# Performance work log

Measured on AMD Instinct MI355X. Metric: run time of the kernel, lower is better.

The kernel has to match this reference:

```python
import jax, jax.numpy as jnp
import numpy as np

CHUNK = 2048   # chunk_size from __init__
EPS = 1e-5     # BatchNorm eps (torch default)


def _proj(x, w, gamma, beta, mean, var):
    # 1x1 conv (no bias) + BatchNorm (eval, running stats) + ReLU
    y = jnp.einsum('bchw,oc->bohw', x, w)
    scale = gamma / jnp.sqrt(var + EPS)
    y = (y - mean[None, :, None, None]) * scale[None, :, None, None] + beta[None, :, None, None]
    return jax.nn.relu(y)


def setup_inputs() -> dict:
    key = jax.random.key(0)
    ks = jax.random.split(key, 8)
    B, Cl, Ci, Co, H, W = 2, 256, 512, 128, 128, 128
    return {
        'lidar_features': jax.random.normal(ks[0], (B, Cl, H, W), jnp.float32),
        'image_features': jax.random.normal(ks[1], (B, Ci, H, W), jnp.float32),
        # kaiming_normal fan_out for 1x1 conv: std = sqrt(2 / Co)
        'lidar_w': jax.random.normal(ks[2], (Co, Cl), jnp.float32) * np.sqrt(2.0 / Co),
        'lidar_gamma': jnp.ones((Co,), jnp.float32),
        'lidar_beta': jnp.zeros((Co,), jnp.float32),
        'lidar_mean': jax.random.normal(ks[3], (Co,), jnp.float32) * 0.1,
        'lidar_var': jax.random.uniform(ks[4], (Co,), jnp.float32, 0.5, 1.5),
        'image_w': jax.random.normal(ks[5], (Co, Ci), jnp.float32) * np.sqrt(2.0 / Co),
        'image_gamma': jnp.ones((Co,), jnp.float32),
        'image_beta': jnp.zeros((Co,), jnp.float32),
        'image_mean': jax.random.normal(ks[6], (Co,), jnp.float32) * 0.1,
        'image_var': jax.random.uniform(ks[7], (Co,), jnp.float32, 0.5, 1.5),
        'modality_weights': jnp.ones((2,), jnp.float32),
    }


def reference(lidar_features, image_features,
              lidar_w, lidar_gamma, lidar_beta, lidar_mean, lidar_var,
              image_w, image_gamma, image_beta, image_mean, image_var,
              modality_weights):
    lidar_proj = _proj(lidar_features, lidar_w, lidar_gamma, lidar_beta, lidar_mean, lidar_var)
    image_proj = _proj(image_features, image_w, image_gamma, image_beta, image_mean, image_var)
    # spatial sizes match by construction, so no interpolation branch
    B, C, H, W = lidar_proj.shape
    P = H * W
    n = P // CHUNK  # P chosen divisible by CHUNK
    # block-diagonal attention: q from image, k=v from lidar, per pixel chunk
    q = image_proj.reshape(B, C, P).transpose(0, 2, 1).reshape(B, n, CHUNK, C)
    k = lidar_proj.reshape(B, C, P).transpose(0, 2, 1).reshape(B, n, CHUNK, C)
    attn = jax.nn.softmax(jnp.einsum('bnqc,bnkc->bnqk', q, k) / jnp.sqrt(jnp.float32(C)), axis=-1)
    out = jnp.einsum('bnqk,bnkc->bnqc', attn, k)  # v == k (both are lidar_proj)
    fused = out.reshape(B, P, C).transpose(0, 2, 1).reshape(B, C, H, W)
    w = jax.nn.softmax(modality_weights)
    return w[0] * image_proj + w[1] * fused
```

## Files before the change

kernel.cpp:

```cpp
#include <hip/hip_runtime.h>
#include <hip/hip_bf16.h>

typedef __attribute__((ext_vector_type(4))) float f32x4;
typedef __attribute__((ext_vector_type(8))) short short8;

#define P_TOT 16384
#define NCO 128
#define EPS 1e-5f
#define ALPHA 0.12752269f

__device__ __forceinline__ unsigned short f2bf(float f) {
  union { float f; unsigned u; } v; v.f = f;
  unsigned r = v.u + 0x7FFFu + ((v.u >> 16) & 1u);
  return (unsigned short)(r >> 16);
}
__device__ __forceinline__ float bf2f(unsigned short h) {
  union { unsigned u; float f; } v; v.u = ((unsigned)h) << 16;
  return v.f;
}
__device__ __forceinline__ unsigned cvtpk_bf16(float lo, float hi) {
  unsigned r;
  asm("v_cvt_pk_bf16_f32 %0, %1, %2" : "=v"(r) : "v"(lo), "v"(hi));
  return r;
}
__device__ __forceinline__ void gload16(const void* g, void* l) {
  __builtin_amdgcn_global_load_lds(
      (const __attribute__((address_space(1))) unsigned*)g,
      (__attribute__((address_space(3))) unsigned*)l, 16, 0, 0);
}

__global__ __launch_bounds__(256) void proj_mfma(
    const float* __restrict__ Xl, const float* __restrict__ Xi,
    const float* __restrict__ Wl, const float* __restrict__ Wi,
    const float* __restrict__ lgm, const float* __restrict__ lbt,
    const float* __restrict__ lmn, const float* __restrict__ lvr,
    const float* __restrict__ igm, const float* __restrict__ ibt,
    const float* __restrict__ imn, const float* __restrict__ ivr,
    unsigned short* __restrict__ Lp, unsigned short* __restrict__ Ip,
    unsigned short* __restrict__ Vg)
{
  __shared__ __align__(16) char smem[36352];
  float* sc_l = (float*)(smem + 35328);
  float* sh_l = (float*)(smem + 35840);

  const int t = threadIdx.x;
  const int w = t >> 6, l = t & 63, l15 = l & 15, g = l >> 4;
  const int zz = blockIdx.y, b = zz & 1, mod = zz >> 1;
  const int pb = blockIdx.x * 128;

  const float* Xg = mod ? Xi : Xl;
  const float* Wg = mod ? Wi : Wl;
  const int Cin = mod ? 512 : 256;
  unsigned short* outp = mod ? Ip : Lp;

  if (t < 128) {
    const float* G = mod ? igm : lgm;
    const float* Bt = mod ? ibt : lbt;
    const float* M = mod ? imn : lmn;
    const float* V = mod ? ivr : lvr;
    float s = G[t] / sqrtf(V[t] + EPS);
    sc_l[t] = s;
    sh_l[t] = Bt[t] - M[t] * s;
  }

  f32x4 o[2][8];
#pragma unroll
  for (int qt = 0; qt < 2; ++qt)
#pragma unroll
    for (int nt = 0; nt < 8; ++nt) o[qt][nt] = (f32x4){0.f, 0.f, 0.f, 0.f};

  uint2 xr[8], wr[8];
  auto load_tiles = [&](int s) {
    int cc = s * 64;
#pragma unroll
    for (int i = 0; i < 8; ++i) {
      int e = t + 256 * i;
      int c = e >> 5, p4 = e & 31;
      f32x4 x = *(const f32x4*)(Xg + ((size_t)(b * Cin + cc + c)) * P_TOT + pb + p4 * 4);
      xr[i].x = cvtpk_bf16(x[0], x[1]);
      xr[i].y = cvtpk_bf16(x[2], x[3]);
    }
#pragma unroll
    for (int i = 0; i < 8; ++i) {
      int e = t + 256 * i;
      int co = e >> 4, c4 = e & 15;
      f32x4 wv = *(const f32x4*)(Wg + (size_t)co * Cin + cc + c4 * 4);
      wr[i].x = cvtpk_bf16(wv[0], wv[1]);
      wr[i].y = cvtpk_bf16(wv[2], wv[3]);
    }
  };

  load_tiles(0);
  const int nsteps = Cin >> 6;
  for (int s = 0; s < nsteps; ++s) {
    __syncthreads();
#pragma unroll
    for (int i = 0; i < 8; ++i) {
      int e = t + 256 * i;
      int c = e >> 5, p4 = e & 31;
      *(uint2*)(smem + c * 264 + p4 * 8) = xr[i];
    }
#pragma unroll
    for (int i = 0; i < 8; ++i) {
      int e = t + 256 * i;
      int co = e >> 4, c4 = e & 15;
      *(uint2*)(smem + 16896 + co * 144 + c4 * 8) = wr[i];
    }
    if (s + 1 < nsteps) load_tiles(s + 1);
    __syncthreads();

#pragma unroll
    for (int kkc = 0; kkc < 2; ++kkc) {
      short8 a[2];
#pragma unroll
      for (int qt = 0; qt < 2; ++qt) {
        const char* ab = smem + (kkc * 32 + g * 8) * 264 + (w * 32 + qt * 16 + l15) * 2;
        union { unsigned uu[4]; short8 v; } cv;
#pragma unroll
        for (int e2 = 0; e2 < 4; ++e2) {
          unsigned lo = *(const unsigned short*)(ab + (2 * e2) * 264);
          unsigned hi = *(const unsigned short*)(ab + (2 * e2 + 1) * 264);
          cv.uu[e2] = lo | (hi << 16);
        }
        a[qt] = cv.v;
      }
#pragma unroll
      for (int nt = 0; nt < 8; ++nt) {
        short8 wf = *(const short8*)(smem + 16896 + (nt * 16 + l15) * 144 + kkc * 64 + g * 16);
        o[0][nt] = __builtin_amdgcn_mfma_f32_16x16x32_bf16(a[0], wf, o[0][nt], 0, 0, 0);
        o[1][nt] = __builtin_amdgcn_mfma_f32_16x16x32_bf16(a[1], wf, o[1][nt], 0, 0, 0);
      }
    }
  }

  __syncthreads();
#pragma unroll
  for (int nt = 0; nt < 8; ++nt) {
    float scv = sc_l[nt * 16 + l15];
    float shv = sh_l[nt * 16 + l15];
#pragma unroll
    for (int qt = 0; qt < 2; ++qt)
#pragma unroll
      for (int r = 0; r < 4; ++r) {
        int p = w * 32 + qt * 16 + 4 * g + r;
        float y = fmaxf(fmaf(o[qt][nt][r], scv, shv), 0.f);
        *(unsigned short*)(smem + p * 272 + (nt * 16 + l15) * 2) = f2bf(y);
      }
  }
  __syncthreads();
  {
    int p = t >> 1, half = t & 1;
    const char* Tb = smem + p * 272 + half * 128;
    unsigned short* ob = outp + ((size_t)b * P_TOT + pb + p) * NCO + half * 64;
#pragma unroll
    for (int i = 0; i < 8; ++i)
      *(uint4*)(ob + i * 8) = *(const uint4*)(Tb + i * 16);
  }
  if (mod == 0) {
    int co = t & 127, ph = t >> 7;
    unsigned short* vb = Vg + ((size_t)b * NCO + co) * P_TOT + pb + ph * 64;
    unsigned pkv[32];
#pragma unroll
    for (int j2 = 0; j2 < 32; ++j2) {
      unsigned lo = *(const unsigned short*)(smem + (ph * 64 + 2 * j2) * 272 + co * 2);
      unsigned hi = *(const unsigned short*)(smem + (ph * 64 + 2 * j2 + 1) * 272 + co * 2);
      pkv[j2] = lo | (hi << 16);
    }
#pragma unroll
    for (int i = 0; i < 8; ++i)
      *(uint4*)(vb + i * 8) = *(const uint4*)&pkv[i * 4];
  }
}

__global__ __launch_bounds__(256) void attn_kernel(
    const unsigned short* __restrict__ Lp,
    const unsigned short* __restrict__ Ip,
    const unsigned short* __restrict__ Vg,
    const float* __restrict__ mw,
    float* __restrict__ out)
{
  __shared__ __align__(16) char smem[65536];

  const int t = threadIdx.x;
  const int w = t >> 6, l = t & 63;
  const int l15 = l & 15, g = l >> 4;
  const int gid = blockIdx.x;
  const int bx = gid >> 4;
  const int chunk = gid & 7;
  const int b = (gid >> 3) & 1;
  const int pq0 = chunk * 2048 + bx * 128;
  const int qw = pq0 + w * 32;

  short8 qf[2][4];
#pragma unroll
  for (int qt = 0; qt < 2; ++qt)
#pragma unroll
    for (int kkc = 0; kkc < 4; ++kkc)
      qf[qt][kkc] = *(const short8*)(Ip +
          ((size_t)b * P_TOT + qw + qt * 16 + l15) * NCO + kkc * 32 + g * 8);

  const char* srcK[4];
  const char* srcV[4];
  int ldsOff[4];
#pragma unroll
  for (int i = 0; i < 4; ++i) {
    int pos = (w * 4 + i) * 4 + (l >> 4);
    int nt = pos >> 4, gp = (pos >> 2) & 3, rr = pos & 3;
    int kp = (nt >> 1) * 32 + gp * 8 + (nt & 1) * 4 + rr;
    srcK[i] = (const char*)Lp +
              ((size_t)b * P_TOT + chunk * 2048 + kp) * 256 +
              (((l & 15) * 16) ^ ((pos & 7) << 4));
    int c = (w * 4 + i) * 8 + (l >> 3);
    srcV[i] = (const char*)Vg +
              ((size_t)(b * NCO + c) * P_TOT + chunk * 2048) * 2 +
              (((l & 7) * 16) ^ ((c & 7) << 4));
    ldsOff[i] = (w * 4 + i) * 1024;
  }

  float m_[2] = {-1e30f, -1e30f}, lsum[2] = {0.f, 0.f};
  f32x4 o[2][8];
#pragma unroll
  for (int qt = 0; qt < 2; ++qt)
#pragma unroll
    for (int ct = 0; ct < 8; ++ct) o[qt][ct] = (f32x4){0.f, 0.f, 0.f, 0.f};

#pragma unroll
  for (int i = 0; i < 4; ++i) {
    gload16(srcK[i], smem + ldsOff[i]);
    gload16(srcV[i], smem + 32768 + ldsOff[i]);
  }
  __syncthreads();

  int cur = 0;
  for (int kt = 0; kt < 32; ++kt) {
    if (kt + 1 < 32) {
#pragma unroll
      for (int i = 0; i < 4; ++i) {
        gload16(srcK[i] + (size_t)(kt + 1) * 16384,
                smem + (cur ^ 1) * 16384 + ldsOff[i]);
        gload16(srcV[i] + (size_t)(kt + 1) * 128,
                smem + 32768 + (cur ^ 1) * 16384 + ldsOff[i]);
      }
    }
    const char* Kb = smem + cur * 16384;
    const char* Vb = smem + 32768 + cur * 16384;

    f32x4 s[2][4];
#pragma unroll
    for (int qt = 0; qt < 2; ++qt)
#pragma unroll
      for (int nt = 0; nt < 4; ++nt) s[qt][nt] = (f32x4){0.f, 0.f, 0.f, 0.f};
#pragma unroll
    for (int kkc = 0; kkc < 4; ++kkc) {
#pragma unroll
      for (int nt = 0; nt < 4; ++nt) {
        short8 kf = *(const short8*)(Kb + (nt * 16 + l15) * 256 +
                        ((kkc * 64 + g * 16) ^ ((l15 & 7) << 4)));
        s[0][nt] = __builtin_amdgcn_mfma_f32_16x16x32_bf16(kf, qf[0][kkc], s[0][nt], 0, 0, 0);
        s[1][nt] = __builtin_amdgcn_mfma_f32_16x16x32_bf16(kf, qf[1][kkc], s[1][nt], 0, 0, 0);
      }
    }

    unsigned pk[2][4][2];
    float f_[2];
    int upd[2];
#pragma unroll
    for (int qt = 0; qt < 2; ++qt) {
      float v0 = fmaxf(fmaxf(s[qt][0][0], s[qt][0][1]), fmaxf(s[qt][0][2], s[qt][0][3]));
      float v1 = fmaxf(fmaxf(s[qt][1][0], s[qt][1][1]), fmaxf(s[qt][1][2], s[qt][1][3]));
      float v2 = fmaxf(fmaxf(s[qt][2][0], s[qt][2][1]), fmaxf(s[qt][2][2], s[qt][2][3]));
      float v3 = fmaxf(fmaxf(s[qt][3][0], s[qt][3][1]), fmaxf(s[qt][3][2], s[qt][3][3]));
      float v = fmaxf(fmaxf(v0, v1), fmaxf(v2, v3));
      v = fmaxf(v, __shfl_xor(v, 16));
      v = fmaxf(v, __shfl_xor(v, 32));
      float pm = v * ALPHA;
      upd[qt] = __any(pm > m_[qt] + 8.f);
      float mn = m_[qt];
      if (upd[qt]) {
        mn = fmaxf(m_[qt], pm);
        f_[qt] = __builtin_amdgcn_exp2f(m_[qt] - mn);
        m_[qt] = mn;
      } else {
        f_[qt] = 1.f;
      }
      float ps = 0.f;
#pragma unroll
      for (int nt = 0; nt < 4; ++nt) {
#pragma unroll
        for (int r = 0; r < 4; ++r) {
          float p = __builtin_amdgcn_exp2f(s[qt][nt][r] * ALPHA - mn);
          s[qt][nt][r] = p;
          ps += p;
        }
        pk[qt][nt][0] = cvtpk_bf16(s[qt][nt][0], s[qt][nt][1]);
        pk[qt][nt][1] = cvtpk_bf16(s[qt][nt][2], s[qt][nt][3]);
      }
      ps += __shfl_xor(ps, 16);
      ps += __shfl_xor(ps, 32);
      lsum[qt] = lsum[qt] * f_[qt] + ps;
    }

#pragma unroll
    for (int qt = 0; qt < 2; ++qt)
      if (upd[qt]) {
#pragma unroll
        for (int r = 0; r < 4; ++r) {
          float fb = __shfl(f_[qt], 20 * g + r);
#pragma unroll
          for (int ct = 0; ct < 8; ++ct) o[qt][ct][r] *= fb;
        }
      }

#pragma unroll
    for (int kk2 = 0; kk2 < 2; ++kk2) {
      short8 af[2];
#pragma unroll
      for (int qt = 0; qt < 2; ++qt) {
        union { unsigned u[4]; short8 v; } x;
        x.u[0] = pk[qt][2 * kk2][0];
        x.u[1] = pk[qt][2 * kk2][1];
        x.u[2] = pk[qt][2 * kk2 + 1][0];
        x.u[3] = pk[qt][2 * kk2 + 1][1];
        af[qt] = x.v;
      }
#pragma unroll
      for (int ct = 0; ct < 8; ++ct) {
        short8 vf = *(const short8*)(Vb + (ct * 16 + l15) * 128 +
                        ((kk2 * 64 + g * 16) ^ ((l15 & 7) << 4)));
        o[0][ct] = __builtin_amdgcn_mfma_f32_16x16x32_bf16(af[0], vf, o[0][ct], 0, 0, 0);
        o[1][ct] = __builtin_amdgcn_mfma_f32_16x16x32_bf16(af[1], vf, o[1][ct], 0, 0, 0);
      }
    }
    __syncthreads();
    cur ^= 1;
  }

  float a0 = mw[0], a1 = mw[1];
  float mx = fmaxf(a0, a1);
  float e0 = __builtin_amdgcn_exp2f((a0 - mx) * 1.442695041f);
  float e1 = __builtin_amdgcn_exp2f((a1 - mx) * 1.442695041f);
  float w0 = e0 / (e0 + e1), w1 = e1 / (e0 + e1);

  float invb[2][4];
#pragma unroll
  for (int qt = 0; qt < 2; ++qt) {
    float inv = w1 / lsum[qt];
#pragma unroll
    for (int r = 0; r < 4; ++r) invb[qt][r] = __shfl(inv, 20 * g + r);
  }

  float (*T)[132] = (float (*)[132])smem;
#pragma unroll
  for (int ch = 0; ch < 2; ++ch) {
    __syncthreads();
#pragma unroll
    for (int qt = 0; qt < 2; ++qt)
#pragma unroll
      for (int c4 = 0; c4 < 4; ++c4) {
        int ct = ch * 4 + c4;
#pragma unroll
        for (int r = 0; r < 4; ++r) {
          int qb = w * 32 + qt * 16 + 4 * g + r;
          float img = bf2f(Ip[((size_t)b * P_TOT + pq0 + qb) * NCO + ct * 16 + l15]);
          T[c4 * 16 + l15][qb] = w0 * img + invb[qt][r] * o[qt][ct][r];
        }
      }
    __syncthreads();
    {
      int c = t >> 2, q0 = (t & 3) * 32;
      float* Ob = out + ((size_t)b * NCO + ch * 64 + c) * P_TOT + pq0 + q0;
#pragma unroll
      for (int i2 = 0; i2 < 8; ++i2)
        *(f32x4*)(Ob + 4 * i2) = *(const f32x4*)&T[c][q0 + 4 * i2];
    }
  }
}

extern "C" void kernel_launch(void* const* d_in, const int* in_sizes, int n_in,
                              void* d_out, int out_size, void* d_ws, size_t ws_size,
                              hipStream_t stream) {
  const float* lidar = (const float*)d_in[0];
  const float* image = (const float*)d_in[1];
  const float* lw = (const float*)d_in[2];
  const float* lg = (const float*)d_in[3];
  const float* lb = (const float*)d_in[4];
  const float* lm = (const float*)d_in[5];
  const float* lv = (const float*)d_in[6];
  const float* iw = (const float*)d_in[7];
  const float* ig = (const float*)d_in[8];
  const float* ibt = (const float*)d_in[9];
  const float* im = (const float*)d_in[10];
  const float* iv = (const float*)d_in[11];
  const float* mw = (const float*)d_in[12];

  unsigned short* Lp = (unsigned short*)d_ws;
  unsigned short* Ip = Lp + (size_t)2 * P_TOT * NCO;
  unsigned short* Vg = Ip + (size_t)2 * P_TOT * NCO;

  dim3 gp(P_TOT / 128, 4);
  proj_mfma<<<gp, 256, 0, stream>>>(lidar, image, lw, iw,
                                    lg, lb, lm, lv, ig, ibt, im, iv,
                                    Lp, Ip, Vg);

  attn_kernel<<<dim3(256), 256, 0, stream>>>(Lp, Ip, Vg, mw, (float*)d_out);
}
```

Before: 97.63 us.

## Split attention keys across two half-blocks and merge softmax partials in LDS

The attention block grows from 256 to 512 threads. Each half processes 1024 of the 2048 keys in its chunk using its own 64KB LDS region, so 128KB of LDS per block. At the end, half 1 writes its partial output, max and sum to shared memory, and half 0 merges them with the online-softmax rescale before adding the image term and storing. This doubles the number of waves working on each query tile to hide latency in a grid of only 256 blocks. In exchange it adds a merge stage, extra barriers and a much larger LDS footprint, which may limit occupancy.

```diff
diff --git a/kernel.cpp b/kernel.cpp
--- a/kernel.cpp
+++ b/kernel.cpp
@@ -172,18 +172,21 @@
   }
 }
 
-__global__ __launch_bounds__(256) void attn_kernel(
+__global__ __launch_bounds__(512) void attn_kernel(
     const unsigned short* __restrict__ Lp,
     const unsigned short* __restrict__ Ip,
     const unsigned short* __restrict__ Vg,
     const float* __restrict__ mw,
     float* __restrict__ out)
 {
-  __shared__ __align__(16) char smem[65536];
+  __shared__ __align__(16) char smem[131072];
 
   const int t = threadIdx.x;
-  const int w = t >> 6, l = t & 63;
+  const int half = t >> 8;
+  const int t2 = t & 255;
+  const int w = t2 >> 6, l = t & 63;
   const int l15 = l & 15, g = l >> 4;
+  const int hb = half << 16;
   const int gid = blockIdx.x;
   const int bx = gid >> 4;
   const int chunk = gid & 7;
@@ -208,13 +211,13 @@
     int nt = pos >> 4, gp = (pos >> 2) & 3, rr = pos & 3;
     int kp = (nt >> 1) * 32 + gp * 8 + (nt & 1) * 4 + rr;
     srcK[i] = (const char*)Lp +
-              ((size_t)b * P_TOT + chunk * 2048 + kp) * 256 +
+              ((size_t)b * P_TOT + chunk * 2048 + half * 1024 + kp) * 256 +
               (((l & 15) * 16) ^ ((pos & 7) << 4));
     int c = (w * 4 + i) * 8 + (l >> 3);
     srcV[i] = (const char*)Vg +
-              ((size_t)(b * NCO + c) * P_TOT + chunk * 2048) * 2 +
+              (((size_t)(b * NCO + c)) * P_TOT + chunk * 2048 + half * 1024) * 2 +
               (((l & 7) * 16) ^ ((c & 7) << 4));
-    ldsOff[i] = (w * 4 + i) * 1024;
+    ldsOff[i] = hb + (w * 4 + i) * 1024;
   }
 
   float m_[2] = {-1e30f, -1e30f}, lsum[2] = {0.f, 0.f};
@@ -232,8 +235,8 @@
   __syncthreads();
 
   int cur = 0;
-  for (int kt = 0; kt < 32; ++kt) {
-    if (kt + 1 < 32) {
+  for (int kt = 0; kt < 16; ++kt) {
+    if (kt + 1 < 16) {
 #pragma unroll
       for (int i = 0; i < 4; ++i) {
         gload16(srcK[i] + (size_t)(kt + 1) * 16384,
@@ -242,8 +245,8 @@
                 smem + 32768 + (cur ^ 1) * 16384 + ldsOff[i]);
       }
     }
-    const char* Kb = smem + cur * 16384;
-    const char* Vb = smem + 32768 + cur * 16384;
+    const char* Kb = smem + hb + cur * 16384;
+    const char* Vb = smem + hb + 32768 + cur * 16384;
 
     f32x4 s[2][4];
 #pragma unroll
@@ -335,43 +338,89 @@
     cur ^= 1;
   }
 
+  float* Tp = (float*)smem;
+  float* m1a = (float*)(smem + 67584);
+  float* l1a = (float*)(smem + 68096);
+
+  if (half == 1) {
+#pragma unroll
+    for (int qt = 0; qt < 2; ++qt) {
+      int qb = w * 32 + qt * 16 + 4 * g;
+#pragma unroll
+      for (int ct = 0; ct < 8; ++ct) {
+        int c = ct * 16 + l15;
+        *(f32x4*)&Tp[c * 132 + qb] = o[qt][ct];
+      }
+      if (g == 0) {
+        m1a[w * 32 + qt * 16 + l15] = m_[qt];
+        l1a[w * 32 + qt * 16 + l15] = lsum[qt];
+      }
+    }
+  }
+  __syncthreads();
+
   float a0 = mw[0], a1 = mw[1];
   float mx = fmaxf(a0, a1);
   float e0 = __builtin_amdgcn_exp2f((a0 - mx) * 1.442695041f);
   float e1 = __builtin_amdgcn_exp2f((a1 - mx) * 1.442695041f);
-  float w0 = e0 / (e0 + e1), w1 = e1 / (e0 + e1);
-
-  float invb[2][4];
-#pragma unroll
-  for (int qt = 0; qt < 2; ++qt) {
-    float inv = w1 / lsum[qt];
-#pragma unroll
-    for (int r = 0; r < 4; ++r) invb[qt][r] = __shfl(inv, 20 * g + r);
-  }
-
-  float (*T)[132] = (float (*)[132])smem;
-#pragma unroll
-  for (int ch = 0; ch < 2; ++ch) {
-    __syncthreads();
-#pragma unroll
-    for (int qt = 0; qt < 2; ++qt)
-#pragma unroll
-      for (int c4 = 0; c4 < 4; ++c4) {
-        int ct = ch * 4 + c4;
+  float w0m = e0 / (e0 + e1), w1m = e1 / (e0 + e1);
+
+  if (half == 0) {
+#pragma unroll
+    for (int qt = 0; qt < 2; ++qt) {
+      int qb = w * 32 + qt * 16 + 4 * g;
+      f32x4 m1v = *(const f32x4*)&m1a[qb];
+      f32x4 l1v = *(const f32x4*)&l1a[qb];
+      float A[4], Bc[4];
+#pragma unroll
+      for (int r = 0; r < 4; ++r) {
+        float m0r = __shfl(m_[qt], 20 * g + r);
+        float l0r = __shfl(lsum[qt], 20 * g + r);
+        float M = fmaxf(m0r, m1v[r]);
+        float w0h = __builtin_amdgcn_exp2f(m0r - M);
+        float w1h = __builtin_amdgcn_exp2f(m1v[r] - M);
+        float L = w0h * l0r + w1h * l1v[r];
+        A[r] = w1m * w0h / L;
+        Bc[r] = w1m * w1h / L;
+      }
+#pragma unroll
+      for (int ct = 0; ct < 8; ++ct) {
+        int c = ct * 16 + l15;
+        f32x4 o1 = *(const f32x4*)&Tp[c * 132 + qb];
+#pragma unroll
+        for (int r = 0; r < 4; ++r)
+          o[qt][ct][r] = A[r] * o[qt][ct][r] + Bc[r] * o1[r];
+      }
+    }
+  }
+  __syncthreads();
+
+  if (half == 0) {
+#pragma unroll
+    for (int qt = 0; qt < 2; ++qt) {
+      int qb = w * 32 + qt * 16 + 4 * g;
+#pragma unroll
+      for (int ct = 0; ct < 8; ++ct) {
+        int c = ct * 16 + l15;
+        f32x4 v = o[qt][ct];
 #pragma unroll
         for (int r = 0; r < 4; ++r) {
-          int qb = w * 32 + qt * 16 + 4 * g + r;
-          float img = bf2f(Ip[((size_t)b * P_TOT + pq0 + qb) * NCO + ct * 16 + l15]);
-          T[c4 * 16 + l15][qb] = w0 * img + invb[qt][r] * o[qt][ct][r];
+          float img = bf2f(Ip[((size_t)b * P_TOT + pq0 + qb + r) * NCO + c]);
+          v[r] = w0m * img + v[r];
         }
-      }
-    __syncthreads();
-    {
-      int c = t >> 2, q0 = (t & 3) * 32;
-      float* Ob = out + ((size_t)b * NCO + ch * 64 + c) * P_TOT + pq0 + q0;
-#pragma unroll
-      for (int i2 = 0; i2 < 8; ++i2)
-        *(f32x4*)(Ob + 4 * i2) = *(const f32x4*)&T[c][q0 + 4 * i2];
+        *(f32x4*)&Tp[c * 132 + qb] = v;
+      }
+    }
+  }
+  __syncthreads();
+  {
+    int cc = t >> 5;
+    int q0 = (t & 31) * 4;
+#pragma unroll
+    for (int i2 = 0; i2 < 8; ++i2) {
+      int c = cc + i2 * 16;
+      float* Ob = out + ((size_t)b * NCO + c) * P_TOT + pq0 + q0;
+      *(f32x4*)Ob = *(const f32x4*)&Tp[c * 132 + q0];
     }
   }
 }
@@ -402,5 +451,5 @@
                                     lg, lb, lm, lv, ig, ibt, im, iv,
                                     Lp, Ip, Vg);
 
-  attn_kernel<<<dim3(256), 256, 0, stream>>>(Lp, Ip, Vg, mw, (float*)d_out);
-}
+  attn_kernel<<<dim3(256), 512, 0, stream>>>(Lp, Ip, Vg, mw, (float*)d_out);
+}
```

After: 81.33 us. 1.2x faster.
